# Performance work log

Hardware: AMD Instinct MI355X
Metric: run time of the kernel (lower is better)

## Reference

```python
import jax, jax.numpy as jnp
import numpy as np

B, NG, FS, D, HH, C = 256, 32, 30, 1024, 3, 1024   # graphs, nodes/graph, feat, embed, heads, per-head dim
EPG = 160                                           # edges per graph
K1, K2, K3 = 26, 13, 4                              # ceil(0.8*32), ceil(0.5*26), ceil(0.3*13)


def gat_conv(x, src, dst, mask, W, a_src, a_dst, bias, N):
    """PyG GATConv (concat heads, negative_slope=0.2, add_self_loops=True), eval mode."""
    loop = jnp.arange(N, dtype=src.dtype)
    s = jnp.concatenate([src, loop])
    d = jnp.concatenate([dst, loop])
    m = jnp.concatenate([mask, jnp.ones((N,), bool)])
    xl = (x @ W).reshape(N, HH, C)                       # [N,H,C]
    al_s = jnp.sum(xl * a_src, -1)                       # [N,H]
    al_d = jnp.sum(xl * a_dst, -1)
    logits = jax.nn.leaky_relu(al_s[s] + al_d[d], negative_slope=0.2)  # [E,H]
    logits = jnp.where(m[:, None], logits, jnp.finfo(x.dtype).min)
    mx = jax.ops.segment_max(logits, d, num_segments=N)  # segment softmax over in-edges
    ex = jnp.where(m[:, None], jnp.exp(logits - mx[d]), 0.0)
    den = jax.ops.segment_sum(ex, d, num_segments=N)
    alpha = ex / den[d]
    out = jax.ops.segment_sum(alpha[:, :, None] * xl[s], d, num_segments=N)  # [N,H,C]
    return out.reshape(N, HH * C) + bias


def topk_pool(x, src, dst, mask, p, n_per, k):
    """PyG TopKPooling: score=tanh((x.p)/||p||); keep top-k per graph; gate kept x by score.
    Uniform graph size n_per -> static k. Dropped edges are masked, not removed."""
    score = jnp.tanh((x @ p) / jnp.linalg.norm(p))           # [B*n_per]
    _, idx = jax.lax.top_k(score.reshape(B, n_per), k)       # [B,k] local indices
    perm = (idx + (jnp.arange(B) * n_per)[:, None]).reshape(-1)
    x_new = x[perm] * score[perm][:, None]                   # [B*k, D]
    new_pos = jnp.full((B * n_per,), -1, jnp.int32).at[perm].set(
        jnp.arange(B * k, dtype=jnp.int32))
    ns, nd = new_pos[src], new_pos[dst]
    m = mask & (ns >= 0) & (nd >= 0)
    return x_new, jnp.where(m, ns, 0), jnp.where(m, nd, 0), m


def setup_inputs() -> dict:
    key = jax.random.key(0)
    ks = jax.random.split(key, 40)
    _n = lambda k, shape, s=0.05: jax.random.normal(k, shape, jnp.float32) * s

    x = jax.random.normal(ks[0], (B * NG, FS), jnp.float32)
    src_l = jax.random.randint(ks[1], (B, EPG), 0, NG)
    dst_l = jax.random.randint(ks[2], (B, EPG), 0, NG)
    offs = (jnp.arange(B) * NG)[:, None]
    edge_index = jnp.stack([(src_l + offs).reshape(-1),
                            (dst_l + offs).reshape(-1)]).astype(jnp.int32)
    batch_index = jnp.repeat(jnp.arange(B), NG).astype(jnp.int32)
    edge_attr = jax.random.normal(ks[3], (B * EPG, 6), jnp.float32)  # unused by model

    d = {"x": x, "edge_attr": edge_attr, "edge_index": edge_index, "batch_index": batch_index}
    ins = [FS, D, D]
    ki = 4
    for i, fin in enumerate(ins, 1):
        d[f"g{i}_W"] = _n(ks[ki], (fin, HH * C)); ki += 1
        d[f"g{i}_as"] = _n(ks[ki], (HH, C)); ki += 1
        d[f"g{i}_ad"] = _n(ks[ki], (HH, C)); ki += 1
        d[f"g{i}_b"] = jnp.zeros((HH * C,), jnp.float32)
        d[f"t{i}_W"] = _n(ks[ki], (HH * C, D)); ki += 1
        d[f"t{i}_b"] = jnp.zeros((D,), jnp.float32)
        d[f"p{i}"] = _n(ks[ki], (D,), 1.0); ki += 1
    d["l1_W"] = _n(ks[ki], (D, 1024)); ki += 1
    d["l1_b"] = jnp.zeros((1024,), jnp.float32)
    d["l2_W"] = _n(ks[ki], (1024, 1)); ki += 1
    d["l2_b"] = jnp.zeros((1,), jnp.float32)
    return d


def reference(x, edge_attr, edge_index, batch_index,
              g1_W, g1_as, g1_ad, g1_b, t1_W, t1_b, p1,
              g2_W, g2_as, g2_ad, g2_b, t2_W, t2_b, p2,
              g3_W, g3_as, g3_ad, g3_b, t3_W, t3_b, p3,
              l1_W, l1_b, l2_W, l2_b):
    src, dst = edge_index[0], edge_index[1]
    mask = jnp.ones(src.shape, bool)

    h = gat_conv(x, src, dst, mask, g1_W, g1_as, g1_ad, g1_b, B * NG)
    h = h @ t1_W + t1_b
    h, src, dst, mask = topk_pool(h, src, dst, mask, p1, NG, K1)
    x1 = h.reshape(B, K1, D).mean(1)                     # gap

    h = gat_conv(h, src, dst, mask, g2_W, g2_as, g2_ad, g2_b, B * K1)
    h = h @ t2_W + t2_b
    h, src, dst, mask = topk_pool(h, src, dst, mask, p2, K1, K2)
    x2 = h.reshape(B, K2, D).mean(1)

    h = gat_conv(h, src, dst, mask, g3_W, g3_as, g3_ad, g3_b, B * K2)
    h = h @ t3_W + t3_b
    h, src, dst, mask = topk_pool(h, src, dst, mask, p3, K2, K3)
    x3 = h.reshape(B, K3, D).mean(1)

    z = x1 + x2 + x3
    z = jax.nn.relu(z @ l1_W + l1_b)                     # dropout off (eval)
    return z @ l2_W + l2_b                               # [B, 1]
```

## Files before the change

kernel.cpp:

```cpp
#include <hip/hip_runtime.h>
#include <cstdint>
#include <cstddef>

#define EPG 160
#define HC  3072
#define DD  1024

typedef _Float16 f16x8 __attribute__((ext_vector_type(8)));
typedef _Float16 f16x2 __attribute__((ext_vector_type(2)));
typedef float    f32x4 __attribute__((ext_vector_type(4)));

__device__ __forceinline__ unsigned fenc(float f){
  unsigned u = __float_as_uint(f);
  return (u & 0x80000000u) ? ~u : (u | 0x80000000u);
}
__device__ __forceinline__ float fdec(unsigned u){
  return (u & 0x80000000u) ? __uint_as_float(u ^ 0x80000000u) : __uint_as_float(~u);
}

__device__ __forceinline__ void gload16(const void* g, void* l) {
  __builtin_amdgcn_global_load_lds((const __attribute__((address_space(1))) void*)g,
                                   (__attribute__((address_space(3))) void*)l, 16, 0, 0);
}

__global__ __launch_bounds__(256) void wtrans_kernel(
    const float* __restrict__ W, _Float16* __restrict__ WTh, _Float16* __restrict__ WTl,
    int K, int Nn)
{
  __shared__ float t[32][33];
  const int tx = threadIdx.x, ty = threadIdx.y;
  const int n0 = blockIdx.x * 32, k0 = blockIdx.y * 32;
  #pragma unroll
  for (int i = 0; i < 4; i++) {
    int k = k0 + ty + i * 8;
    t[ty + i * 8][tx] = (k < K) ? W[(size_t)k * Nn + n0 + tx] : 0.f;
  }
  __syncthreads();
  const int kt = k0 >> 5;
  const int c  = tx >> 3;
  const int w8 = tx & 7;
  #pragma unroll
  for (int i = 0; i < 4; i++) {
    int n = n0 + ty + i * 8;
    float v = t[tx][ty + i * 8];
    _Float16 h = (_Float16)v;
    float r = v - (float)h;
    int c2 = c ^ ((n >> 1) & 3);
    size_t addr = ((size_t)kt * Nn + n) * 32 + c2 * 8 + w8;
    WTh[addr] = h;
    WTl[addr] = (_Float16)r;
  }
}

__global__ __launch_bounds__(256) void xsplit_kernel(
    const float* __restrict__ x, _Float16* __restrict__ ATh, _Float16* __restrict__ ATl, int M)
{
  int r = blockIdx.x * 256 + threadIdx.x;
  if (r >= M) return;
  const float* xr = x + (size_t)r * 30;
  float v[32];
  #pragma unroll
  for (int j = 0; j < 32; j++) v[j] = (j < 30) ? xr[j] : 0.f;
  const int sz = (r >> 1) & 3;
  #pragma unroll
  for (int ch = 0; ch < 4; ch++) {
    int c2 = ch ^ sz;
    f16x8 hh, ll;
    #pragma unroll
    for (int j = 0; j < 8; j++) {
      float vv = v[ch * 8 + j];
      _Float16 hv = (_Float16)vv;
      hh[j] = hv; ll[j] = (_Float16)(vv - (float)hv);
    }
    *(f16x8*)&ATh[(size_t)r * 32 + c2 * 8] = hh;
    *(f16x8*)&ATl[(size_t)r * 32 + c2 * 8] = ll;
  }
}

__global__ __launch_bounds__(256) void mfma_gemm(
    const _Float16* __restrict__ ATh, const _Float16* __restrict__ ATl,
    const _Float16* __restrict__ BTh, const _Float16* __restrict__ BTl,
    const float* __restrict__ bias, float* __restrict__ C,
    int M, int N, int K,
    const float* __restrict__ avs, const float* __restrict__ avd,
    float* __restrict__ alsp, float* __restrict__ aldp,
    const float* __restrict__ pvec, float* __restrict__ scp)
{
  __shared__ __align__(16) char smem[2 * 32768];

  const int gx = N >> 7, gy = M >> 7;
  const int lid = blockIdx.x + gx * blockIdx.y;
  int vx, vy;
  const int G = gy & ~7;
  if (lid < gx * G) {
    const int sub = lid & 7, rest = lid >> 3;
    vx = rest % gx; vy = (rest / gx) * 8 + sub;
  } else {
    const int r = lid - gx * G;
    vx = r % gx; vy = G + r / gx;
  }
  const int brow = vy << 7, bcol = vx << 7;

  const int tid  = threadIdx.x;
  const int lane = tid & 63;
  const int w    = tid >> 6;
  const int wr   = (w >> 1) << 6, wc = (w & 1) << 6;
  const int wn   = w & 1;
  const int fr   = lane & 15, g4 = lane >> 4;

  f32x4 acc[4][4];
  #pragma unroll
  for (int m = 0; m < 4; m++)
    #pragma unroll
    for (int n = 0; n < 4; n++) acc[m][n] = (f32x4)0.0f;

  int aoff[4], boff[4];
  #pragma unroll
  for (int m = 0; m < 4; m++) {
    int r = wr + m * 16 + fr;
    aoff[m] = r * 64 + ((g4 ^ ((r >> 1) & 3)) << 4);
  }
  #pragma unroll
  for (int n = 0; n < 4; n++) {
    int r = wc + n * 16 + fr;
    boff[n] = r * 64 + ((g4 ^ ((r >> 1) & 3)) << 4);
  }

  const int ktiles = (K + 31) >> 5;

#define STAGE(ktv, buf)                                                    \
  do {                                                                     \
    char* bse = (buf);                                                     \
    const size_t ab = ((size_t)(ktv) * M + brow) << 6;                     \
    const size_t bb = ((size_t)(ktv) * N + bcol) << 6;                     \
    const char* gah = (const char*)ATh + ab + tid * 16;                    \
    const char* gal = (const char*)ATl + ab + tid * 16;                    \
    const char* gbh = (const char*)BTh + bb + tid * 16;                    \
    const char* gbl = (const char*)BTl + bb + tid * 16;                    \
    gload16(gah,        bse + tid * 16);                                   \
    gload16(gah + 4096, bse + tid * 16 + 4096);                            \
    gload16(gal,        bse + 8192 + tid * 16);                            \
    gload16(gal + 4096, bse + 8192 + tid * 16 + 4096);                     \
    gload16(gbh,        bse + 16384 + tid * 16);                           \
    gload16(gbh + 4096, bse + 16384 + tid * 16 + 4096);                    \
    gload16(gbl,        bse + 24576 + tid * 16);                           \
    gload16(gbl + 4096, bse + 24576 + tid * 16 + 4096);                    \
  } while (0)

  STAGE(0, smem);
  if (ktiles > 1) STAGE(1, smem + 32768);

  for (int kt = 0; kt < ktiles; kt++) {
    char* curb = smem + ((kt & 1) << 15);
    if (kt + 1 < ktiles) {
      asm volatile("s_waitcnt vmcnt(8)" ::: "memory");
    } else {
      asm volatile("s_waitcnt vmcnt(0)" ::: "memory");
    }
    __builtin_amdgcn_s_barrier();
    asm volatile("" ::: "memory");

    f16x8 ah[4], al[4], bh[4], bl[4];
    #pragma unroll
    for (int n = 0; n < 4; n++) {
      bh[n] = *(const f16x8*)(curb + 16384 + boff[n]);
      bl[n] = *(const f16x8*)(curb + 24576 + boff[n]);
    }
    #pragma unroll
    for (int m = 0; m < 4; m++) {
      ah[m] = *(const f16x8*)(curb + aoff[m]);
      al[m] = *(const f16x8*)(curb + 8192 + aoff[m]);
    }
    asm volatile("s_waitcnt lgkmcnt(0)" ::: "memory");
    __builtin_amdgcn_sched_barrier(0);
    __builtin_amdgcn_s_barrier();
    asm volatile("" ::: "memory");

    if (kt + 2 < ktiles) STAGE(kt + 2, curb);

    __builtin_amdgcn_s_setprio(1);
    #pragma unroll
    for (int m = 0; m < 4; m++) {
      #pragma unroll
      for (int n = 0; n < 4; n++) {
        acc[m][n] = __builtin_amdgcn_mfma_f32_16x16x32_f16(ah[m], bh[n], acc[m][n], 0, 0, 0);
        acc[m][n] = __builtin_amdgcn_mfma_f32_16x16x32_f16(al[m], bh[n], acc[m][n], 0, 0, 0);
        acc[m][n] = __builtin_amdgcn_mfma_f32_16x16x32_f16(ah[m], bl[n], acc[m][n], 0, 0, 0);
      }
    }
    __builtin_amdgcn_s_setprio(0);
    asm volatile("" ::: "memory");
  }
#undef STAGE

  const int crow0 = brow + wr + g4 * 4;
  const int ccol0 = bcol + wc + fr;
  #pragma unroll
  for (int n = 0; n < 4; n++) {
    const int col = ccol0 + n * 16;
    const float bv = bias ? bias[col] : 0.f;
    #pragma unroll
    for (int m = 0; m < 4; m++) {
      const int row = crow0 + m * 16;
      #pragma unroll
      for (int q = 0; q < 4; q++)
        C[(size_t)(row + q) * N + col] = acc[m][n][q] + bv;
    }
  }

  if (alsp) {
    const int h3 = bcol >> 10;
    const int slot = ((bcol & 1023) >> 6) + wn;
    #pragma unroll
    for (int m = 0; m < 4; m++) {
      #pragma unroll
      for (int q = 0; q < 4; q++) {
        float ps = 0.f, pd = 0.f;
        #pragma unroll
        for (int n = 0; n < 4; n++) {
          const int col = ccol0 + n * 16;
          const float v = acc[m][n][q];
          ps += v * avs[col]; pd += v * avd[col];
        }
        #pragma unroll
        for (int mk = 1; mk <= 8; mk <<= 1) {
          ps += __shfl_xor(ps, mk);
          pd += __shfl_xor(pd, mk);
        }
        if (fr == 0) {
          const int row = crow0 + m * 16 + q;
          alsp[row * 48 + h3 * 16 + slot] = ps;
          aldp[row * 48 + h3 * 16 + slot] = pd;
        }
      }
    }
  }
  if (scp) {
    const int slot = (bcol >> 6) + wn;
    #pragma unroll
    for (int m = 0; m < 4; m++) {
      #pragma unroll
      for (int q = 0; q < 4; q++) {
        float pp = 0.f;
        #pragma unroll
        for (int n = 0; n < 4; n++) {
          const int col = ccol0 + n * 16;
          pp += (acc[m][n][q] + bias[col]) * pvec[col];
        }
        #pragma unroll
        for (int mk = 1; mk <= 8; mk <<= 1) pp += __shfl_xor(pp, mk);
        if (fr == 0) scp[(crow0 + m * 16 + q) * 16 + slot] = pp;
      }
    }
  }
}

__global__ __launch_bounds__(256) void sgemm_kernel(
    const float* __restrict__ A, const float* __restrict__ B,
    const float* __restrict__ bias, float* __restrict__ C,
    int M, int N, int K, int relu)
{
  __shared__ float As[16][132];
  __shared__ float Bs[16][132];
  const int tid  = threadIdx.x;
  const int brow = blockIdx.y * 128;
  const int bcol = blockIdx.x * 128;
  const int trow = (tid >> 4) * 8;
  const int tcol = (tid & 15) * 8;
  const int ar = tid >> 2, ac = (tid & 3) * 4;
  const int br = tid >> 5, bc = (tid & 31) * 4;
  float acc[8][8];
  #pragma unroll
  for (int i = 0; i < 8; i++)
    #pragma unroll
    for (int j = 0; j < 8; j++) acc[i][j] = 0.f;
  for (int k0 = 0; k0 < K; k0 += 16) {
    #pragma unroll
    for (int i = 0; i < 2; i++) {
      int r = ar + i * 64;
      const float4 v = *(const float4*)&A[(size_t)(brow + r) * K + k0 + ac];
      As[ac + 0][r] = v.x; As[ac + 1][r] = v.y; As[ac + 2][r] = v.z; As[ac + 3][r] = v.w;
    }
    #pragma unroll
    for (int i = 0; i < 2; i++) {
      int r = br + i * 8;
      *(float4*)&Bs[r][bc] = *(const float4*)&B[(size_t)(k0 + r) * N + bcol + bc];
    }
    __syncthreads();
    #pragma unroll
    for (int kk = 0; kk < 16; kk++) {
      float a[8], b[8];
      *(float4*)&a[0] = *(const float4*)&As[kk][trow];
      *(float4*)&a[4] = *(const float4*)&As[kk][trow + 4];
      *(float4*)&b[0] = *(const float4*)&Bs[kk][tcol];
      *(float4*)&b[4] = *(const float4*)&Bs[kk][tcol + 4];
      #pragma unroll
      for (int i = 0; i < 8; i++)
        #pragma unroll
        for (int j = 0; j < 8; j++) acc[i][j] += a[i] * b[j];
    }
    __syncthreads();
  }
  #pragma unroll
  for (int i = 0; i < 8; i++) {
    const size_t row = (size_t)(brow + trow + i) * N + bcol + tcol;
    #pragma unroll
    for (int j0 = 0; j0 < 8; j0 += 4) {
      float4 v;
      float* pv = &v.x;
      #pragma unroll
      for (int q = 0; q < 4; q++) {
        float t = acc[i][j0 + q];
        if (bias) t += bias[bcol + tcol + j0 + q];
        if (relu) t = t > 0.f ? t : 0.f;
        pv[q] = t;
      }
      *(float4*)&C[row + j0] = v;
    }
  }
}

__global__ __launch_bounds__(256) void norm_kernel(
    const float* __restrict__ p1, const float* __restrict__ p2,
    const float* __restrict__ p3, float* __restrict__ nrm)
{
  const float* p = blockIdx.x == 0 ? p1 : (blockIdx.x == 1 ? p2 : p3);
  __shared__ float red[4];
  int tid = threadIdx.x;
  float s = 0.f;
  for (int i = tid; i < DD; i += 256) { float v = p[i]; s += v * v; }
  #pragma unroll
  for (int off = 32; off; off >>= 1) s += __shfl_down(s, off);
  if ((tid & 63) == 0) red[tid >> 6] = s;
  __syncthreads();
  if (tid == 0) nrm[blockIdx.x] = sqrtf(red[0] + red[1] + red[2] + red[3]);
}

__global__ __launch_bounds__(256) void gat_agg(
    const float* __restrict__ xl, const float* __restrict__ alsp, const float* __restrict__ aldp,
    const int* __restrict__ esrc, const int* __restrict__ edst, const int* __restrict__ emask,
    const float* __restrict__ gbias, _Float16* __restrict__ ATh, _Float16* __restrict__ ATl,
    int npg, int Mtot)
{
  const int g = blockIdx.x;
  const int h = blockIdx.y >> 1;
  const int half = blockIdx.y & 1;
  const int tid = threadIdx.x;
  const int base = g * npg;
  __shared__ float sxl[32 * 512];
  __shared__ float s_as[32], s_ad[32], s_mx[32], s_den[32], s_self[32];
  __shared__ unsigned s_mxu[32];
  __shared__ float s_alpha[EPG];
  __shared__ int s_srcl[EPG];
  __shared__ int s_start[33];
  __shared__ int s_cnt[32], s_cur[32];
  __shared__ int s_list[EPG];

  const int colb = h * DD + (half << 9);
  for (int n = 0; n < npg; n++) {
    *(float2*)&sxl[(n << 9) + (tid << 1)] =
        *(const float2*)&xl[(size_t)(base + n) * HC + colb + (tid << 1)];
  }

  if (tid < npg) {
    const float* ps = alsp + (size_t)(base + tid) * 48 + h * 16;
    const float* pdp = aldp + (size_t)(base + tid) * 48 + h * 16;
    float ss = 0.f, dd2 = 0.f;
    #pragma unroll
    for (int s = 0; s < 16; s++) { ss += ps[s]; dd2 += pdp[s]; }
    s_as[tid] = ss;
    s_ad[tid] = dd2;
    s_mxu[tid] = 0u;
    s_den[tid] = 0.f;
    s_cnt[tid] = 0;
    s_cur[tid] = 0;
  }
  __syncthreads();

  int ok = 0, dl = 0;
  float lg = 0.f;
  if (tid < EPG) {
    int ei = g * EPG + tid;
    ok = emask ? emask[ei] : 1;
    if (ok) {
      int sl = esrc[ei] - base;
      dl = edst[ei] - base;
      s_srcl[tid] = sl;
      float v = s_as[sl] + s_ad[dl];
      lg = v > 0.f ? v : 0.2f * v;
      atomicMax(&s_mxu[dl], fenc(lg));
      atomicAdd(&s_cnt[dl], 1);
    }
  }
  float slg = 0.f;
  if (tid < npg) {
    float v = s_as[tid] + s_ad[tid];
    slg = v > 0.f ? v : 0.2f * v;
    atomicMax(&s_mxu[tid], fenc(slg));
  }
  __syncthreads();

  if (tid < npg) s_mx[tid] = fdec(s_mxu[tid]);
  if (tid == 0) {
    int run = 0;
    for (int n = 0; n < npg; n++) { s_start[n] = run; run += s_cnt[n]; }
    s_start[npg] = run;
  }
  __syncthreads();

  float ex = 0.f;
  if (tid < EPG && ok) {
    ex = expf(lg - s_mx[dl]);
    atomicAdd(&s_den[dl], ex);
    int p = s_start[dl] + atomicAdd(&s_cur[dl], 1);
    s_list[p] = tid;
  }
  if (tid < npg) {
    float e2 = expf(slg - s_mx[tid]);
    s_self[tid] = e2;
    atomicAdd(&s_den[tid], e2);
  }
  __syncthreads();

  if (tid < EPG && ok) s_alpha[tid] = ex / s_den[dl];
  if (tid < npg) s_self[tid] = s_self[tid] / s_den[tid];
  __syncthreads();

  const int c = colb + (tid << 1);
  const float b0 = gbias[c], b1 = gbias[c + 1];
  const int kt = c >> 5;
  const int ch = (c >> 3) & 3;
  const int j2 = c & 7;
  for (int n = 0; n < npg; n++) {
    const float2 v = *(const float2*)&sxl[(n << 9) + (tid << 1)];
    float a0 = s_self[n];
    float ax = a0 * v.x, ay = a0 * v.y;
    const int st = s_start[n], en = s_start[n + 1];
    for (int q = st; q < en; q++) {
      int e = s_list[q];
      float a = s_alpha[e];
      const float2 u = *(const float2*)&sxl[(s_srcl[e] << 9) + (tid << 1)];
      ax += a * u.x; ay += a * u.y;
    }
    ax += b0; ay += b1;
    const int R = base + n;
    const int c2 = ch ^ ((R >> 1) & 3);
    const size_t ad = ((size_t)kt * Mtot + R) * 32 + c2 * 8 + j2;
    f16x2 hh, ll;
    _Float16 h0 = (_Float16)ax; hh[0] = h0; ll[0] = (_Float16)(ax - (float)h0);
    _Float16 h1 = (_Float16)ay; hh[1] = h1; ll[1] = (_Float16)(ay - (float)h1);
    *(f16x2*)&ATh[ad] = hh;
    *(f16x2*)&ATl[ad] = ll;
  }
}

__global__ __launch_bounds__(256) void pool_kernel(
    const float* __restrict__ hbuf, const float* __restrict__ scp,
    const int* __restrict__ cs, const int* __restrict__ cd, const int* __restrict__ cm,
    int npg, int k, int Mnext,
    _Float16* __restrict__ ATh, _Float16* __restrict__ ATl,
    float* __restrict__ gap,
    int* __restrict__ ns, int* __restrict__ nd, int* __restrict__ nm,
    const float* __restrict__ nrm, int stage)
{
  int g = blockIdx.x, tid = threadIdx.x;
  __shared__ float ssc[32];
  __shared__ int sord[32];
  __shared__ int snp[32];
  __shared__ float sgp[2][1024];
  if (tid < npg) {
    const float* sp = scp + (size_t)(g * npg + tid) * 16;
    float s = 0.f;
    #pragma unroll
    for (int q = 0; q < 16; q++) s += sp[q];
    ssc[tid] = tanhf(s / nrm[stage]);
  }
  __syncthreads();
  if (tid == 0) {
    for (int i = 0; i < npg; i++) sord[i] = i;
    for (int i = 1; i < npg; i++) {
      int oi = sord[i]; float v = ssc[oi]; int j = i - 1;
      while (j >= 0 && ssc[sord[j]] < v) { sord[j + 1] = sord[j]; j--; }
      sord[j + 1] = oi;
    }
  }
  __syncthreads();
  if (tid < npg) snp[tid] = -1;
  __syncthreads();
  if (tid < k) snp[sord[tid]] = tid;
  __syncthreads();

  const int col0 = (tid & 127) << 3;
  const int rr = tid >> 7;
  const int kt = col0 >> 5;
  const int ch = (col0 >> 3) & 3;
  float part[8];
  #pragma unroll
  for (int j = 0; j < 8; j++) part[j] = 0.f;
  for (int r = rr; r < k; r += 2) {
    int ol = sord[r];
    float s = ssc[ol];
    const float* hr = hbuf + (size_t)(g * npg + ol) * DD + col0;
    float4 v0 = *(const float4*)hr;
    float4 v1 = *(const float4*)(hr + 4);
    float gv[8] = {v0.x * s, v0.y * s, v0.z * s, v0.w * s,
                   v1.x * s, v1.y * s, v1.z * s, v1.w * s};
    #pragma unroll
    for (int j = 0; j < 8; j++) part[j] += gv[j];
    if (ATh) {
      int R = g * k + r;
      int c2 = ch ^ ((R >> 1) & 3);
      size_t ad = ((size_t)kt * Mnext + R) * 32 + c2 * 8;
      f16x8 hh, ll;
      #pragma unroll
      for (int j = 0; j < 8; j++) {
        _Float16 hv = (_Float16)gv[j];
        hh[j] = hv; ll[j] = (_Float16)(gv[j] - (float)hv);
      }
      *(f16x8*)&ATh[ad] = hh;
      *(f16x8*)&ATl[ad] = ll;
    }
  }
  #pragma unroll
  for (int j = 0; j < 8; j++) sgp[rr][col0 + j] = part[j];
  __syncthreads();
  const float fk = (float)k;
  #pragma unroll
  for (int j = 0; j < 4; j++) {
    int cc = tid * 4 + j;
    gap[(size_t)g * DD + cc] = (sgp[0][cc] + sgp[1][cc]) / fk;
  }

  for (int e = tid; e < EPG; e += 256) {
    int ei = g * EPG + e;
    int ok = cm ? cm[ei] : 1;
    int m2 = 0, a = 0, b2 = 0;
    if (ok) {
      int sl = cs[ei] - g * npg, dl = cd[ei] - g * npg;
      int nsl = snp[sl], ndl = snp[dl];
      if (nsl >= 0 && ndl >= 0) { m2 = 1; a = g * k + nsl; b2 = g * k + ndl; }
    }
    ns[ei] = a; nd[ei] = b2; nm[ei] = m2;
  }
}

__global__ __launch_bounds__(256) void zadd_kernel(
    const float* __restrict__ a, const float* __restrict__ b,
    const float* __restrict__ c, float* __restrict__ o)
{
  int i = blockIdx.x * 256 + threadIdx.x;
  o[i] = a[i] + b[i] + c[i];
}

__global__ __launch_bounds__(256) void l2_kernel(
    const float* __restrict__ z2, const float* __restrict__ w,
    const float* __restrict__ b, float* __restrict__ out)
{
  int row = (blockIdx.x * 256 + threadIdx.x) >> 6;
  int lane = threadIdx.x & 63;
  if (row >= 256) return;
  const float* r = z2 + (size_t)row * DD;
  float s = 0.f;
  #pragma unroll 4
  for (int i = lane; i < DD; i += 64) s += r[i] * w[i];
  #pragma unroll
  for (int off = 32; off; off >>= 1) s += __shfl_down(s, off);
  if (lane == 0) out[row] = s + b[0];
}

extern "C" void kernel_launch(void* const* d_in, const int* in_sizes, int n_in,
                              void* d_out, int out_size, void* d_ws, size_t ws_size,
                              hipStream_t stream)
{
  (void)in_sizes; (void)n_in; (void)out_size; (void)ws_size;
  const float* x    = (const float*)d_in[0];
  const int*   eidx = (const int*)d_in[2];
  const float* g1W = (const float*)d_in[4];
  const float* g1as= (const float*)d_in[5];
  const float* g1ad= (const float*)d_in[6];
  const float* g1b = (const float*)d_in[7];
  const float* t1W = (const float*)d_in[8];
  const float* t1b = (const float*)d_in[9];
  const float* p1  = (const float*)d_in[10];
  const float* g2W = (const float*)d_in[11];
  const float* g2as= (const float*)d_in[12];
  const float* g2ad= (const float*)d_in[13];
  const float* g2b = (const float*)d_in[14];
  const float* t2W = (const float*)d_in[15];
  const float* t2b = (const float*)d_in[16];
  const float* p2  = (const float*)d_in[17];
  const float* g3W = (const float*)d_in[18];
  const float* g3as= (const float*)d_in[19];
  const float* g3ad= (const float*)d_in[20];
  const float* g3b = (const float*)d_in[21];
  const float* t3W = (const float*)d_in[22];
  const float* t3b = (const float*)d_in[23];
  const float* p3  = (const float*)d_in[24];
  const float* l1W = (const float*)d_in[25];
  const float* l1b = (const float*)d_in[26];
  const float* l2W = (const float*)d_in[27];
  const float* l2b = (const float*)d_in[28];
  float* outp = (float*)d_out;

  float* W = (float*)d_ws;
  size_t o = 0;
  float* bufA = W + o; o += (size_t)8192 * HC;
  float* bufB = W + o; o += (size_t)8192 * DD;
  _Float16* ATh = (_Float16*)(W + o); o += (size_t)96 * 8192 * 32 / 2;
  _Float16* ATl = (_Float16*)(W + o); o += (size_t)96 * 8192 * 32 / 2;
  float* ALSp = W + o; o += 8192 * 48;
  float* ALDp = W + o; o += 8192 * 48;
  float* SCp  = W + o; o += 8192 * 16;
  float* NRM = W + o; o += 4;
  float* X1  = W + o; o += 256 * DD;
  float* X2  = W + o; o += 256 * DD;
  float* X3  = W + o; o += 256 * DD;
  float* ZB  = W + o; o += 256 * DD;
  float* Z2  = W + o; o += 256 * DD;
  int* E0s = (int*)(W + o); o += 40960;
  int* E0d = (int*)(W + o); o += 40960;
  int* E0m = (int*)(W + o); o += 40960;
  int* E1s = (int*)(W + o); o += 40960;
  int* E1d = (int*)(W + o); o += 40960;
  int* E1m = (int*)(W + o); o += 40960;
  _Float16* WTH = (_Float16*)(W + o); o += (3200 * 1024) / 2;
  _Float16* WTL = (_Float16*)(W + o); o += (3200 * 1024) / 2;

  const int* es1 = eidx;
  const int* ed1 = eidx + 40960;

  norm_kernel<<<3, 256, 0, stream>>>(p1, p2, p3, NRM);

  xsplit_kernel<<<32, 256, 0, stream>>>(x, ATh, ATl, 8192);
  wtrans_kernel<<<dim3(96, 1), dim3(32, 8), 0, stream>>>(g1W, WTH, WTL, 30, HC);
  mfma_gemm<<<dim3(24, 64), 256, 0, stream>>>(ATh, ATl, WTH, WTL, nullptr, bufA, 8192, HC, 30,
                                              g1as, g1ad, ALSp, ALDp, nullptr, nullptr);
  gat_agg<<<dim3(256, 6), 256, 0, stream>>>(bufA, ALSp, ALDp, es1, ed1, nullptr, g1b,
                                            ATh, ATl, 32, 8192);
  wtrans_kernel<<<dim3(32, 96), dim3(32, 8), 0, stream>>>(t1W, WTH, WTL, HC, DD);
  mfma_gemm<<<dim3(8, 64), 256, 0, stream>>>(ATh, ATl, WTH, WTL, t1b, bufB, 8192, DD, HC,
                                             nullptr, nullptr, nullptr, nullptr, p1, SCp);
  pool_kernel<<<256, 256, 0, stream>>>(bufB, SCp, es1, ed1, nullptr, 32, 26, 6656,
                                       ATh, ATl, X1, E0s, E0d, E0m, NRM, 0);

  wtrans_kernel<<<dim3(96, 32), dim3(32, 8), 0, stream>>>(g2W, WTH, WTL, DD, HC);
  mfma_gemm<<<dim3(24, 52), 256, 0, stream>>>(ATh, ATl, WTH, WTL, nullptr, bufA, 6656, HC, DD,
                                              g2as, g2ad, ALSp, ALDp, nullptr, nullptr);
  gat_agg<<<dim3(256, 6), 256, 0, stream>>>(bufA, ALSp, ALDp, E0s, E0d, E0m, g2b,
                                            ATh, ATl, 26, 6656);
  wtrans_kernel<<<dim3(32, 96), dim3(32, 8), 0, stream>>>(t2W, WTH, WTL, HC, DD);
  mfma_gemm<<<dim3(8, 52), 256, 0, stream>>>(ATh, ATl, WTH, WTL, t2b, bufB, 6656, DD, HC,
                                             nullptr, nullptr, nullptr, nullptr, p2, SCp);
  pool_kernel<<<256, 256, 0, stream>>>(bufB, SCp, E0s, E0d, E0m, 26, 13, 3328,
                                       ATh, ATl, X2, E1s, E1d, E1m, NRM, 1);

  wtrans_kernel<<<dim3(96, 32), dim3(32, 8), 0, stream>>>(g3W, WTH, WTL, DD, HC);
  mfma_gemm<<<dim3(24, 26), 256, 0, stream>>>(ATh, ATl, WTH, WTL, nullptr, bufA, 3328, HC, DD,
                                              g3as, g3ad, ALSp, ALDp, nullptr, nullptr);
  gat_agg<<<dim3(256, 6), 256, 0, stream>>>(bufA, ALSp, ALDp, E1s, E1d, E1m, g3b,
                                            ATh, ATl, 13, 3328);
  wtrans_kernel<<<dim3(32, 96), dim3(32, 8), 0, stream>>>(t3W, WTH, WTL, HC, DD);
  mfma_gemm<<<dim3(8, 26), 256, 0, stream>>>(ATh, ATl, WTH, WTL, t3b, bufB, 3328, DD, HC,
                                             nullptr, nullptr, nullptr, nullptr, p3, SCp);
  pool_kernel<<<256, 256, 0, stream>>>(bufB, SCp, E1s, E1d, E1m, 13, 4, 1024,
                                       nullptr, nullptr, X3, E0s, E0d, E0m, NRM, 2);

  zadd_kernel<<<1024, 256, 0, stream>>>(X1, X2, X3, ZB);
  sgemm_kernel<<<dim3(8, 2), 256, 0, stream>>>(ZB, l1W, l1b, Z2, 256, DD, DD, 1);
  l2_kernel<<<64, 256, 0, stream>>>(Z2, l2W, l2b, outp);
}
```

Before: 1.030 ms.

## Fuse head zadd, l1 GEMM+relu and l2 dot into one kernel

The separate sum, 256x1024x1024 SGEMM and final dot-product kernels are replaced by a single head kernel. Each block sums X1+X2+X3 for 4 rows into LDS, computes 256 l1 output columns, applies relu and multiplies by l2W, then reduces to per-block partials. A tiny second kernel adds the four partials and the bias. This removes the intermediate ZB/Z2 buffers and a launch, and raises parallelism from 16 blocks to 256, at the cost of re-reading l1W once per row group.

```diff
diff --git a/kernel.cpp b/kernel.cpp
--- a/kernel.cpp
+++ b/kernel.cpp
@@ -255,71 +255,6 @@
   }
 }
 
-__global__ __launch_bounds__(256) void sgemm_kernel(
-    const float* __restrict__ A, const float* __restrict__ B,
-    const float* __restrict__ bias, float* __restrict__ C,
-    int M, int N, int K, int relu)
-{
-  __shared__ float As[16][132];
-  __shared__ float Bs[16][132];
-  const int tid  = threadIdx.x;
-  const int brow = blockIdx.y * 128;
-  const int bcol = blockIdx.x * 128;
-  const int trow = (tid >> 4) * 8;
-  const int tcol = (tid & 15) * 8;
-  const int ar = tid >> 2, ac = (tid & 3) * 4;
-  const int br = tid >> 5, bc = (tid & 31) * 4;
-  float acc[8][8];
-  #pragma unroll
-  for (int i = 0; i < 8; i++)
-    #pragma unroll
-    for (int j = 0; j < 8; j++) acc[i][j] = 0.f;
-  for (int k0 = 0; k0 < K; k0 += 16) {
-    #pragma unroll
-    for (int i = 0; i < 2; i++) {
-      int r = ar + i * 64;
-      const float4 v = *(const float4*)&A[(size_t)(brow + r) * K + k0 + ac];
-      As[ac + 0][r] = v.x; As[ac + 1][r] = v.y; As[ac + 2][r] = v.z; As[ac + 3][r] = v.w;
-    }
-    #pragma unroll
-    for (int i = 0; i < 2; i++) {
-      int r = br + i * 8;
-      *(float4*)&Bs[r][bc] = *(const float4*)&B[(size_t)(k0 + r) * N + bcol + bc];
-    }
-    __syncthreads();
-    #pragma unroll
-    for (int kk = 0; kk < 16; kk++) {
-      float a[8], b[8];
-      *(float4*)&a[0] = *(const float4*)&As[kk][trow];
-      *(float4*)&a[4] = *(const float4*)&As[kk][trow + 4];
-      *(float4*)&b[0] = *(const float4*)&Bs[kk][tcol];
-      *(float4*)&b[4] = *(const float4*)&Bs[kk][tcol + 4];
-      #pragma unroll
-      for (int i = 0; i < 8; i++)
-        #pragma unroll
-        for (int j = 0; j < 8; j++) acc[i][j] += a[i] * b[j];
-    }
-    __syncthreads();
-  }
-  #pragma unroll
-  for (int i = 0; i < 8; i++) {
-    const size_t row = (size_t)(brow + trow + i) * N + bcol + tcol;
-    #pragma unroll
-    for (int j0 = 0; j0 < 8; j0 += 4) {
-      float4 v;
-      float* pv = &v.x;
-      #pragma unroll
-      for (int q = 0; q < 4; q++) {
-        float t = acc[i][j0 + q];
-        if (bias) t += bias[bcol + tcol + j0 + q];
-        if (relu) t = t > 0.f ? t : 0.f;
-        pv[q] = t;
-      }
-      *(float4*)&C[row + j0] = v;
-    }
-  }
-}
-
 __global__ __launch_bounds__(256) void norm_kernel(
     const float* __restrict__ p1, const float* __restrict__ p2,
     const float* __restrict__ p3, float* __restrict__ nrm)
@@ -544,28 +479,64 @@
   }
 }
 
-__global__ __launch_bounds__(256) void zadd_kernel(
-    const float* __restrict__ a, const float* __restrict__ b,
-    const float* __restrict__ c, float* __restrict__ o)
-{
-  int i = blockIdx.x * 256 + threadIdx.x;
-  o[i] = a[i] + b[i] + c[i];
-}
-
-__global__ __launch_bounds__(256) void l2_kernel(
-    const float* __restrict__ z2, const float* __restrict__ w,
-    const float* __restrict__ b, float* __restrict__ out)
-{
-  int row = (blockIdx.x * 256 + threadIdx.x) >> 6;
-  int lane = threadIdx.x & 63;
-  if (row >= 256) return;
-  const float* r = z2 + (size_t)row * DD;
-  float s = 0.f;
-  #pragma unroll 4
-  for (int i = lane; i < DD; i += 64) s += r[i] * w[i];
-  #pragma unroll
-  for (int off = 32; off; off >>= 1) s += __shfl_down(s, off);
-  if (lane == 0) out[row] = s + b[0];
+__global__ __launch_bounds__(256) void head_kernel(
+    const float* __restrict__ X1, const float* __restrict__ X2, const float* __restrict__ X3,
+    const float* __restrict__ l1W, const float* __restrict__ l1b,
+    const float* __restrict__ l2W, float* __restrict__ partial)
+{
+  __shared__ float a[4][1024];
+  __shared__ float red[4][4];
+  const int tid = threadIdx.x;
+  const int cg = blockIdx.x, rg = blockIdx.y;
+  const int row0 = rg << 2;
+  #pragma unroll
+  for (int r = 0; r < 4; r++) {
+    const size_t ro = (size_t)(row0 + r) << 10;
+    #pragma unroll
+    for (int jj = 0; jj < 4; jj++) {
+      int j = tid + jj * 256;
+      a[r][j] = X1[ro + j] + X2[ro + j] + X3[ro + j];
+    }
+  }
+  __syncthreads();
+
+  const int col = (cg << 8) + tid;
+  float acc0 = 0.f, acc1 = 0.f, acc2 = 0.f, acc3 = 0.f;
+  #pragma unroll 8
+  for (int k = 0; k < 1024; k++) {
+    float wv = l1W[((size_t)k << 10) + col];
+    acc0 += a[0][k] * wv;
+    acc1 += a[1][k] * wv;
+    acc2 += a[2][k] * wv;
+    acc3 += a[3][k] * wv;
+  }
+  const float bv = l1b[col], lw = l2W[col];
+  float v0 = fmaxf(acc0 + bv, 0.f) * lw;
+  float v1 = fmaxf(acc1 + bv, 0.f) * lw;
+  float v2 = fmaxf(acc2 + bv, 0.f) * lw;
+  float v3 = fmaxf(acc3 + bv, 0.f) * lw;
+  #pragma unroll
+  for (int off = 32; off; off >>= 1) {
+    v0 += __shfl_down(v0, off);
+    v1 += __shfl_down(v1, off);
+    v2 += __shfl_down(v2, off);
+    v3 += __shfl_down(v3, off);
+  }
+  const int lane = tid & 63, wid = tid >> 6;
+  if (lane == 0) { red[wid][0] = v0; red[wid][1] = v1; red[wid][2] = v2; red[wid][3] = v3; }
+  __syncthreads();
+  if (tid < 4)
+    partial[(size_t)(row0 + tid) * 4 + cg] =
+        red[0][tid] + red[1][tid] + red[2][tid] + red[3][tid];
+}
+
+__global__ __launch_bounds__(256) void head2_kernel(
+    const float* __restrict__ partial, const float* __restrict__ l2b,
+    float* __restrict__ out)
+{
+  int r = threadIdx.x;
+  out[r] = partial[r * 4 + 0] + partial[r * 4 + 1] +
+           partial[r * 4 + 2] + partial[r * 4 + 3] + l2b[0];
 }
 
 extern "C" void kernel_launch(void* const* d_in, const int* in_sizes, int n_in,
@@ -615,8 +586,7 @@
   float* X1  = W + o; o += 256 * DD;
   float* X2  = W + o; o += 256 * DD;
   float* X3  = W + o; o += 256 * DD;
-  float* ZB  = W + o; o += 256 * DD;
-  float* Z2  = W + o; o += 256 * DD;
+  float* HP  = W + o; o += 256 * 4;
   int* E0s = (int*)(W + o); o += 40960;
   int* E0d = (int*)(W + o); o += 40960;
   int* E0m = (int*)(W + o); o += 40960;
@@ -665,7 +635,6 @@
   pool_kernel<<<256, 256, 0, stream>>>(bufB, SCp, E1s, E1d, E1m, 13, 4, 1024,
                                        nullptr, nullptr, X3, E0s, E0d, E0m, NRM, 2);
 
-  zadd_kernel<<<1024, 256, 0, stream>>>(X1, X2, X3, ZB);
-  sgemm_kernel<<<dim3(8, 2), 256, 0, stream>>>(ZB, l1W, l1b, Z2, 256, DD, DD, 1);
-  l2_kernel<<<64, 256, 0, stream>>>(Z2, l2W, l2b, outp);
-}
+  head_kernel<<<dim3(4, 64), 256, 0, stream>>>(X1, X2, X3, l1W, l1b, l2W, HP);
+  head2_kernel<<<1, 256, 0, stream>>>(HP, l2b, outp);
+}
```

After: 954.1 us. 1.08x faster.
